# Performance work log

Measured on AMD Instinct MI355X. Metric: run time of the kernel, lower is better.

## Reference

```python
import jax, jax.numpy as jnp
import numpy as np

B, S, D, H = 2, 2048, 1024, 16
DH = D // H
SCALE = 1.0 / np.sqrt(D).astype(np.float32)  # module uses sqrt(d_model), not sqrt(d_h)


def setup_inputs() -> dict:
    key = jax.random.key(0)
    ks = jax.random.split(key, 11)
    def lin(k):
        kw, kb = jax.random.split(k)
        W = jax.random.normal(kw, (D, D), jnp.float32) * 0.02
        b = jax.random.normal(kb, (D,), jnp.float32) * 0.02
        return W, b
    Wq, bq = lin(ks[0]); Wk, bk = lin(ks[1]); Wv, bv = lin(ks[2]); Wo, bo = lin(ks[3])
    Q = jax.random.normal(ks[4], (B, S, D), jnp.float32)
    K = jax.random.normal(ks[5], (B, S, D), jnp.float32)
    V = jax.random.normal(ks[6], (B, S, D), jnp.float32)
    mask = jnp.triu(jnp.ones((S, S), jnp.bool_), k=1)  # True = masked (causal)
    return {"Q": Q, "K": K, "V": V, "mask": mask,
            "Wq": Wq, "bq": bq, "Wk": Wk, "bk": bk,
            "Wv": Wv, "bv": bv, "Wo": Wo, "bo": bo}


def reference(Q, K, V, mask, Wq, bq, Wk, bk, Wv, bv, Wo, bo):
    # Linear projections (torch Linear: x @ W^T + b; W here stored pre-transposed)
    q = Q @ Wq + bq  # [B,S,D]
    k = K @ Wk + bk
    v = V @ Wv + bv
    # Faithful (scrambled) head split: transpose then reshape for Q and K
    qh = jnp.transpose(q, (0, 2, 1)).reshape(B, H, S, DH)
    kh = jnp.transpose(jnp.transpose(k, (0, 2, 1)).reshape(B, H, S, DH), (0, 1, 3, 2))  # [B,H,DH,S]
    score = jax.nn.softmax(jnp.matmul(qh, kh) * SCALE, axis=-1)  # [B,H,S,S]
    # Faithful post-softmax masking
    score = jnp.where(mask, jnp.float32(-1e9), score)
    # V is reshaped directly (no transpose) per the source
    att = jnp.matmul(score, v.reshape(B, H, S, DH))  # [B,H,S,DH]
    att = att.reshape(B, S, D)
    return att @ Wo + bo  # dropout is identity in eval
```

## Files before the change

### kernel.cpp

```cpp
#include <hip/hip_runtime.h>
#include <hip/hip_bf16.h>


typedef __hip_bfloat16 bf16;
typedef __attribute__((ext_vector_type(8))) short bf16x8;
typedef __attribute__((ext_vector_type(8))) unsigned short u16x8;
typedef __attribute__((ext_vector_type(4))) float f32x4;
typedef __attribute__((address_space(1))) const unsigned int guint;
typedef __attribute__((address_space(3))) unsigned int luint;

constexpr size_t OFF_WCUMT = 0;
constexpr size_t OFF_WVT   = 524288;
constexpr size_t OFF_VB    = 1048576;
constexpr size_t OFF_VVB   = 3145728;
constexpr size_t OFF_SUFB  = 5242880;
constexpr size_t OFF_WOSB  = 5373952;
constexpr size_t OFF_BVF   = 5406720;
constexpr size_t OFF_FLAG  = 5407744;

__device__ __forceinline__ float toF(bf16 x) { return __bfloat162float(x); }
__device__ __forceinline__ unsigned short f2b_bits(float f) {
    unsigned u = __float_as_uint(f);
    return (unsigned short)((u + 0x7FFF + ((u >> 16) & 1)) >> 16);
}

__global__ __launch_bounds__(256) void detect_dtype(const unsigned short* __restrict__ Vraw,
                                                    int* __restrict__ flag) {
    __shared__ int cnt[256];
    const int t = threadIdx.x;
    int weird = 0;
    #pragma unroll
    for (int j = 0; j < 8; ++j) {
        unsigned short h = Vraw[2 * (t * 8 + j)];
        int e = (h >> 7) & 0xFF;
        bool w = (e >= 127 + 21) || (e != 0 && e <= 127 - 21) ||
                 (e == 0 && (h & 0x7F));
        weird += w ? 1 : 0;
    }
    cnt[t] = weird;
    __syncthreads();
    #pragma unroll
    for (int s = 128; s > 0; s >>= 1) {
        if (t < s) cnt[t] += cnt[t + s];
        __syncthreads();
    }
    if (t == 0) *flag = (cnt[0] < 512) ? 1 : 0;
}

__global__ __launch_bounds__(256) void prep(const float* __restrict__ Vf,
                                            const void* __restrict__ WvR,
                                            const void* __restrict__ WoR,
                                            const void* __restrict__ bvR,
                                            bf16* __restrict__ Vb,
                                            bf16* __restrict__ WvT,
                                            bf16* __restrict__ WcumT,
                                            bf16* __restrict__ WoSumTb,
                                            float* __restrict__ bvf,
                                            const int* __restrict__ flag) {
    const int f  = *flag;
    const int bx = blockIdx.x;
    __shared__ unsigned short tile[64][65];

    if (bx < 4096) {
        if (f != 0) return;
        const int i = bx * 256 + threadIdx.x;
        float4 v = ((const float4*)Vf)[i];
        ushort4 h;
        h.x = f2b_bits(v.x); h.y = f2b_bits(v.y);
        h.z = f2b_bits(v.z); h.w = f2b_bits(v.w);
        ((ushort4*)Vb)[i] = h;
        return;
    }
    if (bx < 4352) {
        const int b = bx - 4096;
        const int bi = b >> 4, bj = b & 15;
        const int lane = threadIdx.x & 63, r4 = threadIdx.x >> 6;
        if (f == 1) {
            const unsigned short* src = (const unsigned short*)WvR;
            #pragma unroll
            for (int rr = r4; rr < 64; rr += 4)
                tile[rr][lane] = src[(size_t)(bi * 64 + rr) * 1024 + bj * 64 + lane];
        } else {
            const float* src = (const float*)WvR;
            #pragma unroll
            for (int rr = r4; rr < 64; rr += 4)
                tile[rr][lane] = f2b_bits(src[(size_t)(bi * 64 + rr) * 1024 + bj * 64 + lane]);
        }
        __syncthreads();
        #pragma unroll
        for (int rr = r4; rr < 64; rr += 4)
            ((unsigned short*)WvT)[(size_t)(bj * 64 + rr) * 1024 + bi * 64 + lane] =
                tile[lane][rr];
        return;
    }
    const int fb = bx - 4352;
    if (fb == 16) {
        for (int i = threadIdx.x; i < 1024; i += 256)
            bvf[i] = f ? toF(((const bf16*)bvR)[i]) : ((const float*)bvR)[i];
        return;
    }
    const int lane = threadIdx.x & 63;
    const int g    = threadIdx.x >> 6;
    const int a    = fb * 64 + lane;
    float acc[16];
    #pragma unroll
    for (int j = 0; j < 16; ++j) acc[j] = 0.f;
    for (int q = 0; q < 16; ++q) {
        u16x8 h0, h1;
        #pragma unroll
        for (int j = 0; j < 8; ++j) { h0[j] = f2b_bits(acc[j]); h1[j] = f2b_bits(acc[8 + j]); }
        *(u16x8*)(WcumT + (size_t)a * 1024 + q * 64 + g * 16)     = h0;
        *(u16x8*)(WcumT + (size_t)a * 1024 + q * 64 + g * 16 + 8) = h1;
        #pragma unroll
        for (int j = 0; j < 16; ++j) {
            const int row = q * 64 + g * 16 + j;
            acc[j] += f ? toF(((const bf16*)WoR)[(size_t)row * 1024 + a])
                        : ((const float*)WoR)[(size_t)row * 1024 + a];
        }
    }
    u16x8 h0, h1;
    #pragma unroll
    for (int j = 0; j < 8; ++j) { h0[j] = f2b_bits(acc[j]); h1[j] = f2b_bits(acc[8 + j]); }
    *(u16x8*)(WoSumTb + (size_t)a * 64 + g * 16)     = h0;
    *(u16x8*)(WoSumTb + (size_t)a * 64 + g * 16 + 8) = h1;
}

__global__ __launch_bounds__(512) void foldsuf(const bf16* __restrict__ Vvb,
                                               bf16* __restrict__ sufb) {
    __shared__ float foldrow[128][64];
    const int bh = blockIdx.x;
    const size_t rowbase = (size_t)bh * 128;
    const int t   = threadIdx.x;
    const int r   = t >> 2;
    const int dh0 = (t & 3) * 16;
    float p[16];
    #pragma unroll
    for (int j = 0; j < 16; ++j) p[j] = 0.f;
    const unsigned short* rp = (const unsigned short*)(Vvb + (rowbase + r) * 1024);
    #pragma unroll
    for (int q = 0; q < 16; ++q) {
        u16x8 h0 = *(const u16x8*)(rp + q * 64 + dh0);
        u16x8 h1 = *(const u16x8*)(rp + q * 64 + dh0 + 8);
        #pragma unroll
        for (int j = 0; j < 8; ++j) {
            p[j]     += __uint_as_float((unsigned)(unsigned short)h0[j] << 16);
            p[8 + j] += __uint_as_float((unsigned)(unsigned short)h1[j] << 16);
        }
    }
    #pragma unroll
    for (int j = 0; j < 16; ++j) foldrow[r][dh0 + j] = p[j];
    __syncthreads();
    if (t < 64) {
        float a = 0.f;
        for (int rr = 127; rr >= 0; --rr) {
            sufb[(rowbase + rr) * 64 + t] = __float2bfloat16(a);
            a += foldrow[rr][t];
        }
    }
}

template <int FUSED>
__global__ __launch_bounds__(512, 2)
void mfma8(const bf16* __restrict__ A0, const bf16* __restrict__ A0a,
           const bf16* __restrict__ A1, int lda0, int lda1,
           const bf16* __restrict__ B0, const bf16* __restrict__ B1,
           int ldb0, int ldb1,
           int ksplit, int K,
           const float* __restrict__ biasf, const void* __restrict__ boR,
           void* __restrict__ Cout,
           const int* __restrict__ flag) {
    const int fl = *flag;
    const bf16* A0s = (fl == 1) ? A0 : A0a;
    __shared__ __align__(16) char ldsb[98304];

    const int tid  = threadIdx.x;
    const int lane = tid & 63;
    const int wv   = tid >> 6;
    const int wr   = wv >> 2, wc = wv & 3;

    const int gx = gridDim.x;
    int lin = blockIdx.y * gx + blockIdx.x;
    const int nwg = gx * gridDim.y;
    { const int per = nwg >> 3; lin = (lin & 7) * per + (lin >> 3); }
    const int m0 = (lin / gx) * 128;
    const int n0 = (lin % gx) * 128;

    const int c0row = tid >> 3;
    const int c0k   = 8 * ((tid & 7) ^ (c0row & 7));
    const int c1row = c0row + 64;
    const int c1k   = 8 * ((tid & 7) ^ (c1row & 7));
    const int wb0   = wv * 1024;
    const int wb1   = 8192 + wv * 1024;

    auto stage = [&](int t, int d) {
        const int kb = t << 6;
        const bf16 *Aseg, *Bseg; int ka, la, lb;
        if (kb < ksplit) { Aseg = A0s; Bseg = B0; ka = kb;          la = lda0; lb = ldb0; }
        else             { Aseg = A1;  Bseg = B1; ka = kb - ksplit; la = lda1; lb = ldb1; }
        const int db = d * 32768;
        __builtin_amdgcn_global_load_lds((guint*)(Aseg + (size_t)(m0 + c0row) * la + ka + c0k),
                                         (luint*)(ldsb + db + wb0), 16, 0, 0);
        __builtin_amdgcn_global_load_lds((guint*)(Bseg + (size_t)(n0 + c0row) * lb + ka + c0k),
                                         (luint*)(ldsb + db + 16384 + wb0), 16, 0, 0);
        __builtin_amdgcn_global_load_lds((guint*)(Aseg + (size_t)(m0 + c1row) * la + ka + c1k),
                                         (luint*)(ldsb + db + wb1), 16, 0, 0);
        __builtin_amdgcn_global_load_lds((guint*)(Bseg + (size_t)(n0 + c1row) * lb + ka + c1k),
                                         (luint*)(ldsb + db + 16384 + wb1), 16, 0, 0);
    };

    const int row16 = lane & 15;
    const int arow  = (wr * 64 + row16) * 128;
    const int brow  = (wc * 32 + row16) * 128;
    const int kx    = (lane & 7) << 4;
    const int koff0 = (((lane >> 4) << 4)) ^ kx;
    const int koff1 = (64 | ((lane >> 4) << 4)) ^ kx;

    f32x4 acc[4][2];
    #pragma unroll
    for (int i = 0; i < 4; ++i)
        #pragma unroll
        for (int j = 0; j < 2; ++j)
            acc[i][j] = (f32x4){0.f, 0.f, 0.f, 0.f};

    const int nt = K >> 6;
    stage(0, 0);
    stage(1, 1);
    asm volatile("s_waitcnt vmcnt(4)" ::: "memory");
    __builtin_amdgcn_s_barrier();

    int bufc = 0;
    for (int t = 0; t < nt; ++t) {
        if (t + 2 < nt) {
            int b2 = bufc + 2; if (b2 >= 3) b2 -= 3;
            stage(t + 2, b2);
        }
        const char* Ab = ldsb + bufc * 32768;
        const char* Bb = Ab + 16384;
        #pragma unroll
        for (int ks = 0; ks < 2; ++ks) {
            const int ko = ks ? koff1 : koff0;
            bf16x8 af[4], bf2[2];
            #pragma unroll
            for (int i = 0; i < 4; ++i)
                af[i] = *(const bf16x8*)(Ab + arow + i * 2048 + ko);
            #pragma unroll
            for (int j = 0; j < 2; ++j)
                bf2[j] = *(const bf16x8*)(Bb + brow + j * 2048 + ko);
            #pragma unroll
            for (int i = 0; i < 4; ++i)
                #pragma unroll
                for (int j = 0; j < 2; ++j)
                    acc[i][j] = __builtin_amdgcn_mfma_f32_16x16x32_bf16(
                        af[i], bf2[j], acc[i][j], 0, 0, 0);
        }
        if (t + 1 < nt) {
            if (t + 2 < nt)
                asm volatile("s_waitcnt vmcnt(4)" ::: "memory");
            else
                asm volatile("s_waitcnt vmcnt(0)" ::: "memory");
            __builtin_amdgcn_s_barrier();
        }
        if (++bufc == 3) bufc = 0;
    }

    const int crow0 = (lane >> 4) * 4;
    if (FUSED) {
        float bo_[2]; int nn[2];
        #pragma unroll
        for (int j = 0; j < 2; ++j) {
            const int n = n0 + wc * 32 + j * 16 + row16;
            nn[j]  = n;
            bo_[j] = (fl == 1) ? toF(((const bf16*)boR)[n]) : ((const float*)boR)[n];
        }
        #pragma unroll
        for (int i = 0; i < 4; ++i)
            #pragma unroll
            for (int r = 0; r < 4; ++r) {
                const int m = m0 + wr * 64 + i * 16 + crow0 + r;
                #pragma unroll
                for (int j = 0; j < 2; ++j) {
                    const float res = bo_[j] - 1e9f * acc[i][j][r];
                    if (fl == 1)
                        ((bf16*)Cout)[(size_t)m * 1024 + nn[j]] = __float2bfloat16(res);
                    else
                        ((float*)Cout)[(size_t)m * 1024 + nn[j]] = res;
                }
            }
    } else {
        float bb[2];
        #pragma unroll
        for (int j = 0; j < 2; ++j) {
            const int n = n0 + wc * 32 + j * 16 + row16;
            bb[j] = biasf ? biasf[n] : 0.f;
        }
        #pragma unroll
        for (int i = 0; i < 4; ++i)
            #pragma unroll
            for (int r = 0; r < 4; ++r) {
                const int m = m0 + wr * 64 + i * 16 + crow0 + r;
                bf16* cp = (bf16*)Cout + (size_t)m * 1024 + n0 + wc * 32 + row16;
                #pragma unroll
                for (int j = 0; j < 2; ++j)
                    cp[j * 16] = __float2bfloat16(acc[i][j][r] + bb[j]);
            }
    }
}


extern "C" void kernel_launch(void* const* d_in, const int* in_sizes, int n_in,
                              void* d_out, int out_size, void* d_ws, size_t ws_size,
                              hipStream_t stream) {
    float* ws = (float*)d_ws;
    int* flag = (int*)(ws + OFF_FLAG);

    bf16*  WcumT   = (bf16*)(ws + OFF_WCUMT);
    bf16*  WvT     = (bf16*)(ws + OFF_WVT);
    bf16*  Vb      = (bf16*)(ws + OFF_VB);
    bf16*  Vvb     = (bf16*)(ws + OFF_VVB);
    bf16*  sufb    = (bf16*)(ws + OFF_SUFB);
    bf16*  WoSumTb = (bf16*)(ws + OFF_WOSB);
    float* bvf     = ws + OFF_BVF;

    detect_dtype<<<1, 256, 0, stream>>>((const unsigned short*)d_in[2], flag);
    prep<<<4369, 256, 0, stream>>>((const float*)d_in[2], d_in[8], d_in[10],
                                   d_in[9], Vb, WvT, WcumT, WoSumTb, bvf, flag);
    mfma8<0><<<dim3(8, 32), 512, 0, stream>>>((const bf16*)d_in[2], Vb,
                                              Vb, 1024, 1024,
                                              WvT, WvT, 1024, 1024,
                                              1024, 1024,
                                              bvf, nullptr, Vvb, flag);
    foldsuf<<<32, 512, 0, stream>>>(Vvb, sufb);
    mfma8<1><<<dim3(8, 32), 512, 0, stream>>>(Vvb, Vvb, sufb, 1024, 64,
                                              WcumT, WoSumTb, 1024, 64,
                                              1024, 1088,
                                              nullptr, d_in[11], d_out, flag);
}
```

Before: 173.9 us.

## Split K across wave halves with 64x64 warp tiles and LDS reduction

Reorganizes the 8 waves of each 128x128 GEMM block into two groups of four. Each wave now computes a 64x64 sub-tile over half of every 64-wide K step, instead of a 64x32 tile over the full step. The aim is better fragment reuse: each wave does 16 MFMAs per 8 LDS fragment loads instead of 16 per 12. The two partial accumulators are combined through LDS after the main loop, which adds two barriers, 64 KB of LDS traffic, and an epilogue run by only half the waves. Doubling the accumulator registers also raises register pressure under launch_bounds(512,2).

After: 176.3 us. No clear change (+1.4%).

```diff
diff --git a/kernel.cpp b/kernel.cpp
--- a/kernel.cpp
+++ b/kernel.cpp
@@ -176,7 +176,9 @@
     const int tid  = threadIdx.x;
     const int lane = tid & 63;
     const int wv   = tid >> 6;
-    const int wr   = wv >> 2, wc = wv & 3;
+    const int sub  = wv & 3;
+    const int wr   = sub >> 1, wc = sub & 1;
+    const int khalf= wv >> 2;
 
     const int gx = gridDim.x;
     int lin = blockIdx.y * gx + blockIdx.x;
@@ -210,16 +212,17 @@
 
     const int row16 = lane & 15;
     const int arow  = (wr * 64 + row16) * 128;
-    const int brow  = (wc * 32 + row16) * 128;
+    const int brow  = (wc * 64 + row16) * 128;
     const int kx    = (lane & 7) << 4;
     const int koff0 = (((lane >> 4) << 4)) ^ kx;
     const int koff1 = (64 | ((lane >> 4) << 4)) ^ kx;
-
-    f32x4 acc[4][2];
+    const int ko    = khalf ? koff1 : koff0;
+
+    f32x4 acc[4][4];
     #pragma unroll
     for (int i = 0; i < 4; ++i)
         #pragma unroll
-        for (int j = 0; j < 2; ++j)
+        for (int j = 0; j < 4; ++j)
             acc[i][j] = (f32x4){0.f, 0.f, 0.f, 0.f};
 
     const int nt = K >> 6;
@@ -236,23 +239,19 @@
         }
         const char* Ab = ldsb + bufc * 32768;
         const char* Bb = Ab + 16384;
-        #pragma unroll
-        for (int ks = 0; ks < 2; ++ks) {
-            const int ko = ks ? koff1 : koff0;
-            bf16x8 af[4], bf2[2];
-            #pragma unroll
-            for (int i = 0; i < 4; ++i)
-                af[i] = *(const bf16x8*)(Ab + arow + i * 2048 + ko);
-            #pragma unroll
-            for (int j = 0; j < 2; ++j)
-                bf2[j] = *(const bf16x8*)(Bb + brow + j * 2048 + ko);
-            #pragma unroll
-            for (int i = 0; i < 4; ++i)
-                #pragma unroll
-                for (int j = 0; j < 2; ++j)
-                    acc[i][j] = __builtin_amdgcn_mfma_f32_16x16x32_bf16(
-                        af[i], bf2[j], acc[i][j], 0, 0, 0);
-        }
+        bf16x8 af[4], bfv[4];
+        #pragma unroll
+        for (int i = 0; i < 4; ++i)
+            af[i] = *(const bf16x8*)(Ab + arow + i * 2048 + ko);
+        #pragma unroll
+        for (int j = 0; j < 4; ++j)
+            bfv[j] = *(const bf16x8*)(Bb + brow + j * 2048 + ko);
+        #pragma unroll
+        for (int i = 0; i < 4; ++i)
+            #pragma unroll
+            for (int j = 0; j < 4; ++j)
+                acc[i][j] = __builtin_amdgcn_mfma_f32_16x16x32_bf16(
+                    af[i], bfv[j], acc[i][j], 0, 0, 0);
         if (t + 1 < nt) {
             if (t + 2 < nt)
                 asm volatile("s_waitcnt vmcnt(4)" ::: "memory");
@@ -263,12 +262,35 @@
         if (++bufc == 3) bufc = 0;
     }
 
+    __syncthreads();
+    if (wv >= 4) {
+        float* ex = (float*)ldsb + (size_t)sub * 4096;
+        #pragma unroll
+        for (int i = 0; i < 4; ++i)
+            #pragma unroll
+            for (int j = 0; j < 4; ++j)
+                *(f32x4*)(ex + (i * 4 + j) * 256 + lane * 4) = acc[i][j];
+    }
+    __syncthreads();
+    if (wv >= 4) return;
+    {
+        const float* ex = (const float*)ldsb + (size_t)sub * 4096;
+        #pragma unroll
+        for (int i = 0; i < 4; ++i)
+            #pragma unroll
+            for (int j = 0; j < 4; ++j) {
+                f32x4 o = *(const f32x4*)(ex + (i * 4 + j) * 256 + lane * 4);
+                acc[i][j][0] += o[0]; acc[i][j][1] += o[1];
+                acc[i][j][2] += o[2]; acc[i][j][3] += o[3];
+            }
+    }
+
     const int crow0 = (lane >> 4) * 4;
     if (FUSED) {
-        float bo_[2]; int nn[2];
-        #pragma unroll
-        for (int j = 0; j < 2; ++j) {
-            const int n = n0 + wc * 32 + j * 16 + row16;
+        float bo_[4]; int nn[4];
+        #pragma unroll
+        for (int j = 0; j < 4; ++j) {
+            const int n = n0 + wc * 64 + j * 16 + row16;
             nn[j]  = n;
             bo_[j] = (fl == 1) ? toF(((const bf16*)boR)[n]) : ((const float*)boR)[n];
         }
@@ -278,7 +300,7 @@
             for (int r = 0; r < 4; ++r) {
                 const int m = m0 + wr * 64 + i * 16 + crow0 + r;
                 #pragma unroll
-                for (int j = 0; j < 2; ++j) {
+                for (int j = 0; j < 4; ++j) {
                     const float res = bo_[j] - 1e9f * acc[i][j][r];
                     if (fl == 1)
                         ((bf16*)Cout)[(size_t)m * 1024 + nn[j]] = __float2bfloat16(res);
@@ -287,10 +309,10 @@
                 }
             }
     } else {
-        float bb[2];
-        #pragma unroll
-        for (int j = 0; j < 2; ++j) {
-            const int n = n0 + wc * 32 + j * 16 + row16;
+        float bb[4];
+        #pragma unroll
+        for (int j = 0; j < 4; ++j) {
+            const int n = n0 + wc * 64 + j * 16 + row16;
             bb[j] = biasf ? biasf[n] : 0.f;
         }
         #pragma unroll
@@ -298,9 +320,9 @@
             #pragma unroll
             for (int r = 0; r < 4; ++r) {
                 const int m = m0 + wr * 64 + i * 16 + crow0 + r;
-                bf16* cp = (bf16*)Cout + (size_t)m * 1024 + n0 + wc * 32 + row16;
+                bf16* cp = (bf16*)Cout + (size_t)m * 1024 + n0 + wc * 64 + row16;
                 #pragma unroll
-                for (int j = 0; j < 2; ++j)
+                for (int j = 0; j < 4; ++j)
                     cp[j * 16] = __float2bfloat16(acc[i][j][r] + bb[j]);
             }
     }
```
